# Performance work log

Measured on AMD Instinct MI355X. Metric: run time of the kernel, lower is better.

Reference implementation:

```python
import jax, jax.numpy as jnp
import numpy as np

D, N, F_IN, F_OUT = 2, 4096, 128, 128
DENSITY = 0.005  # avg degree ~20 per row in the 0/1 attention graphs
NEG_INF = -1e30


def setup_inputs() -> dict:
    key = jax.random.key(0)
    ks = jax.random.split(key, 12)
    X = jax.random.normal(ks[0], (D, N, F_IN), dtype=jnp.float32)
    # Dense Laplacian operator used in torch.sparse.mm(L[i], h_p); scaled so tanh stays non-degenerate
    L = jax.random.normal(ks[1], (D, N, N), dtype=jnp.float32) / np.float32(np.sqrt(N))
    # Upper/lower adjacency: 0/1 matrices (GATLayer extracts edges via adj == 1)
    L_u = (jax.random.uniform(ks[2], (D, N, N)) < DENSITY).astype(jnp.float32)
    L_d = (jax.random.uniform(ks[3], (D, N, N)) < DENSITY).astype(jnp.float32)
    s = np.float32(0.05)
    Wp = jax.random.normal(ks[4], (D, F_IN, F_OUT), dtype=jnp.float32) * s
    Ws = jax.random.normal(ks[5], (D, F_IN, F_OUT), dtype=jnp.float32) * s
    Wu = jax.random.normal(ks[6], (D, F_IN, F_OUT), dtype=jnp.float32) * s
    au1 = jax.random.normal(ks[7], (D, F_OUT), dtype=jnp.float32) * s
    au2 = jax.random.normal(ks[8], (D, F_OUT), dtype=jnp.float32) * s
    Wd = jax.random.normal(ks[9], (D, F_IN, F_OUT), dtype=jnp.float32) * s
    ad1 = jax.random.normal(ks[10], (D, F_OUT), dtype=jnp.float32) * s
    ad2 = jax.random.normal(ks[11], (D, F_OUT), dtype=jnp.float32) * s
    return {"X": X, "L": L, "L_u": L_u, "L_d": L_d,
            "Wp": Wp, "Ws": Ws, "Wu": Wu, "au1": au1, "au2": au2,
            "Wd": Wd, "ad1": ad1, "ad2": ad2, "dimensions": D}


def _gat(x, adj, W, a1, a2):
    # GATLayer.forward with boundary=False: linear -> edge scores -> LeakyReLU ->
    # row-wise softmax restricted to adj==1 entries -> sparse mm.
    h = x @ W                                   # [N, F_OUT]
    s1 = h @ a1                                 # [N]  (a_1 linear, bias=False)
    s2 = h @ a2                                 # [N]
    scores = jax.nn.leaky_relu(s1[:, None] + s2[None, :])  # [N, N], slope 0.01
    mask = adj == 1.0
    scores = jnp.where(mask, scores, NEG_INF)
    attn = jax.nn.softmax(scores, axis=1)
    attn = jnp.where(mask, attn, 0.0)           # zero rows with no edges (sparse softmax semantics)
    return attn @ h                             # [N, F_OUT]


def _san_dim(x, L, Lu, Ld, Wp, Ws, Wu, au1, au2, Wd, ad1, ad2):
    h_p = jnp.tanh(L @ (x @ Wp))
    h_s = jnp.tanh(x @ Ws)
    h_u = jnp.tanh(_gat(x, Lu, Wu, au1, au2))
    h_d = jnp.tanh(_gat(x, Ld, Wd, ad1, ad2))
    return h_s + h_u + h_d + h_p


def reference(X, L, L_u, L_d, Wp, Ws, Wu, au1, au2, Wd, ad1, ad2, dimensions):
    # vmap over the `dimensions` simplex levels (all per-level params stacked on axis 0)
    return jax.vmap(_san_dim)(X, L, L_u, L_d, Wp, Ws, Wu, au1, au2, Wd, ad1, ad2)
```

## Files before the change

### kernel.cpp

```cpp
#include <hip/hip_runtime.h>
#include <hip/hip_bf16.h>

#define NN 4096
#define FD 128
#define NDIM 2
#define CAP 256

typedef unsigned long long u64;

#define OFF_HMAT 0
#define OFF_SVEC 3145728
#define OFF_HP   3178496
#define OFF_H0T  7372800
#define OFF_MASK 7897088

typedef _Float16 f16x8 __attribute__((ext_vector_type(8)));
typedef float f32x4 __attribute__((ext_vector_type(4)));
typedef float f32x4v __attribute__((ext_vector_type(4)));
typedef unsigned long long u64x2 __attribute__((ext_vector_type(2)));

union P4 { _Float16 h[4]; int2 i2; };

__device__ __forceinline__ float f4get(const float4& v, int j) {
    return j == 0 ? v.x : j == 1 ? v.y : j == 2 ? v.z : v.w;
}

__global__ __launch_bounds__(256) void k_xw(
    const float* __restrict__ X, const float* __restrict__ Wp,
    const float* __restrict__ Wsm, const float* __restrict__ Wu,
    const float* __restrict__ Wd, float* __restrict__ hmat,
    _Float16* __restrict__ h0T) {
  int d = blockIdx.z, p = blockIdx.y;
  int r0 = blockIdx.x * 128;
  const float* W = (p == 0 ? Wp : p == 1 ? Wsm : p == 2 ? Wu : Wd) + (size_t)d * FD * FD;
  const float* Xd = X + ((size_t)d * NN + r0) * FD;
  __shared__ int4 As4[2048];
  __shared__ int4 Bs4[2048];
  char* As = (char*)As4; char* Bs = (char*)Bs4;
  int t = threadIdx.x;

#pragma unroll 4
  for (int u = 0; u < 16; u++) {
    int id = t + u * 256;
    int row = id >> 5, k4 = (id & 31) * 4;
    float4 v = *(const float4*)(Xd + (size_t)row * FD + k4);
    P4 pk;
    pk.h[0] = (_Float16)v.x; pk.h[1] = (_Float16)v.y;
    pk.h[2] = (_Float16)v.z; pk.h[3] = (_Float16)v.w;
    int off = (row * 256 + k4 * 2) ^ ((row & 7) << 4);
    *(int2*)(As + off) = pk.i2;
  }
#pragma unroll 4
  for (int u = 0; u < 16; u++) {
    int id = t + u * 256;
    int k = id >> 5, n4 = (id & 31) * 4;
    float4 v = *(const float4*)(W + (size_t)k * FD + n4);
#pragma unroll
    for (int j = 0; j < 4; j++) {
      int n = n4 + j;
      int off = (n * 256 + k * 2) ^ ((n & 7) << 4);
      *(_Float16*)(Bs + off) = (_Float16)f4get(v, j);
    }
  }
  __syncthreads();

  int w = t >> 6, l = t & 63;
  int lr = l & 15, lkb = (l >> 4) * 16;
  f32x4 acc[2][8] = {};
#pragma unroll
  for (int kb = 0; kb < 4; kb++) {
    f16x8 a[2], b[8];
#pragma unroll
    for (int m = 0; m < 2; m++) {
      int row = w * 32 + m * 16 + lr;
      int off = (row * 256 + kb * 64 + lkb) ^ ((row & 7) << 4);
      a[m] = *(const f16x8*)(As + off);
    }
#pragma unroll
    for (int n = 0; n < 8; n++) {
      int rn = n * 16 + lr;
      int off = (rn * 256 + kb * 64 + lkb) ^ ((rn & 7) << 4);
      b[n] = *(const f16x8*)(Bs + off);
    }
#pragma unroll
    for (int m = 0; m < 2; m++)
#pragma unroll
      for (int n = 0; n < 8; n++)
        acc[m][n] = __builtin_amdgcn_mfma_f32_16x16x32_f16(a[m], b[n], acc[m][n], 0, 0, 0);
  }

  if (p == 0) {
    _Float16* hT = h0T + (size_t)d * FD * NN;
#pragma unroll
    for (int m = 0; m < 2; m++)
#pragma unroll
      for (int n = 0; n < 8; n++) {
        int col = n * 16 + lr;
        int grow = r0 + w * 32 + m * 16 + (l >> 4) * 4;
        P4 pk;
#pragma unroll
        for (int r = 0; r < 4; r++) pk.h[r] = (_Float16)acc[m][n][r];
        *(int2*)(hT + (size_t)col * NN + grow) = pk.i2;
      }
  } else {
    float* o = hmat + ((size_t)(d * 3 + p - 1) * NN + r0) * FD;
#pragma unroll
    for (int m = 0; m < 2; m++)
#pragma unroll
      for (int n = 0; n < 8; n++)
#pragma unroll
        for (int r = 0; r < 4; r++)
          o[(size_t)(w * 32 + m * 16 + (l >> 4) * 4 + r) * FD + n * 16 + lr] = acc[m][n][r];
  }
}

__global__ __launch_bounds__(256) void k_svec(
    const float* __restrict__ hmat, const float* __restrict__ au1,
    const float* __restrict__ au2, const float* __restrict__ ad1,
    const float* __restrict__ ad2, float* __restrict__ svec) {
  int v = blockIdx.y, d = blockIdx.z;
  int w = threadIdx.x >> 6, lane = threadIdx.x & 63;
  int i = blockIdx.x * 4 + w;
  const float* a = (v == 0 ? au1 : v == 1 ? au2 : v == 2 ? ad1 : ad2) + (size_t)d * FD;
  const float* h = hmat + ((size_t)(d * 3 + 1 + (v >> 1)) * NN + i) * FD;
  float x = h[lane] * a[lane] + h[64 + lane] * a[64 + lane];
#pragma unroll
  for (int o = 1; o < 64; o <<= 1) x += __shfl_xor(x, o);
  if (lane == 0) svec[(size_t)(d * 4 + v) * NN + i] = x;
}

__global__ __launch_bounds__(256) void k_mega(
    const float* __restrict__ L, const _Float16* __restrict__ h0T,
    float* __restrict__ hp,
    const float* __restrict__ Lu, const float* __restrict__ Ldn,
    u64* __restrict__ mask) {
  __shared__ int4 sm4[1536];
  int t = threadIdx.x, w = t >> 6, lane = t & 63;

  if (blockIdx.x < 512) {
    int b = blockIdx.x;
    int r0 = (b & 63) * 64, ks = (b >> 6) & 3, d = b >> 8;
    const float* Lr = L + (size_t)d * NN * NN;
    const _Float16* hT = h0T + (size_t)d * FD * NN;
    char* As = (char*)sm4;
    char* Bs = (char*)(sm4 + 512);
    int lr = lane & 15, lkb = (lane >> 4) * 16;
    f32x4 acc[8] = {};
    int kbeg = ks * 1024;
    for (int kk = kbeg; kk < kbeg + 1024; kk += 64) {
#pragma unroll
      for (int u = 0; u < 4; u++) {
        int id = t + u * 256;
        int row = id >> 4, k4 = (id & 15) * 4;
        f32x4v v = __builtin_nontemporal_load(
            (const f32x4v*)(Lr + (size_t)(r0 + row) * NN + kk) + (k4 >> 2));
        P4 pk;
        pk.h[0] = (_Float16)v[0]; pk.h[1] = (_Float16)v[1];
        pk.h[2] = (_Float16)v[2]; pk.h[3] = (_Float16)v[3];
        int off = (row * 128 + k4 * 2) ^ ((row & 7) << 4);
        *(int2*)(As + off) = pk.i2;
      }
#pragma unroll
      for (int u = 0; u < 4; u++) {
        int id = t + u * 256;
        int n = id >> 3, k8 = (id & 7) * 8;
        int4 v = *(const int4*)(hT + (size_t)n * NN + kk + k8);
        int off = (n * 128 + k8 * 2) ^ ((n & 7) << 4);
        *(int4*)(Bs + off) = v;
      }
      __syncthreads();
#pragma unroll
      for (int kb = 0; kb < 2; kb++) {
        int row = w * 16 + lr;
        int offA = (row * 128 + kb * 64 + lkb) ^ ((row & 7) << 4);
        f16x8 a = *(const f16x8*)(As + offA);
        f16x8 bb[8];
#pragma unroll
        for (int n = 0; n < 8; n++) {
          int rn = n * 16 + lr;
          int off = (rn * 128 + kb * 64 + lkb) ^ ((rn & 7) << 4);
          bb[n] = *(const f16x8*)(Bs + off);
        }
#pragma unroll
        for (int n = 0; n < 8; n++)
          acc[n] = __builtin_amdgcn_mfma_f32_16x16x32_f16(a, bb[n], acc[n], 0, 0, 0);
      }
      __syncthreads();
    }
    float* o = hp + ((size_t)(d * 4 + ks) * NN + r0) * FD;
#pragma unroll
    for (int n = 0; n < 8; n++)
#pragma unroll
      for (int r = 0; r < 4; r++)
        o[(size_t)(w * 16 + (lane >> 4) * 4 + r) * FD + n * 16 + lr] = acc[n][r];
    return;
  }

  int hr = (blockIdx.x - 512) * 4 + w;
  int p = hr >> 13;
  int rq = hr & 8191;
  int row = rq >> 1, half = rq & 1;
  const float* src = ((p & 1) ? Ldn : Lu) +
                     ((size_t)(p >> 1) * NN + row) * (size_t)NN + half * 2048;
  f32x4v v[8];
#pragma unroll
  for (int q = 0; q < 4; q++) {
    const f32x4v* s4 = (const f32x4v*)(src + q * 512);
    v[2 * q]     = __builtin_nontemporal_load(s4 + lane);
    v[2 * q + 1] = __builtin_nontemporal_load(s4 + 64 + lane);
  }
  u64* o = mask + ((size_t)p * NN + row) * 64 + half * 32;
#pragma unroll
  for (int q = 0; q < 4; q++) {
    u64 m0 = __ballot(v[2 * q][0] == 1.0f);
    u64 m1 = __ballot(v[2 * q][1] == 1.0f);
    u64 m2 = __ballot(v[2 * q][2] == 1.0f);
    u64 m3 = __ballot(v[2 * q][3] == 1.0f);
    u64 m4 = __ballot(v[2 * q + 1][0] == 1.0f);
    u64 m5 = __ballot(v[2 * q + 1][1] == 1.0f);
    u64 m6 = __ballot(v[2 * q + 1][2] == 1.0f);
    u64 m7 = __ballot(v[2 * q + 1][3] == 1.0f);
    if (lane == 0) {
      u64x2 a0 = {m0, m1}, a1 = {m2, m3}, a2 = {m4, m5}, a3 = {m6, m7};
      __builtin_nontemporal_store(a0, (u64x2*)(o + q * 8 + 0));
      __builtin_nontemporal_store(a1, (u64x2*)(o + q * 8 + 2));
      __builtin_nontemporal_store(a2, (u64x2*)(o + q * 8 + 4));
      __builtin_nontemporal_store(a3, (u64x2*)(o + q * 8 + 6));
    }
  }
}

__global__ __launch_bounds__(256) void k_gatc(
    const u64* __restrict__ mask, const float* __restrict__ hmat,
    const float* __restrict__ svec, const float* __restrict__ hp,
    float* __restrict__ out) {
  int d = blockIdx.y;
  int w = threadIdx.x >> 6, lane = threadIdx.x & 63;
  int i = blockIdx.x * 4 + w;

  __shared__ int ej[4][2][CAP];
  __shared__ float wt[4][2][CAP];

  float ga[2][2];
#pragma unroll
  for (int a = 0; a < 2; a++) {
    const u64* mrow = mask + ((size_t)((d * 2 + a) * NN) + i) * 64;
    const float* h = hmat + (size_t)(d * 3 + 1 + a) * NN * FD;
    const float* s1 = svec + (size_t)(d * 4 + 2 * a) * NN;
    const float* s2 = svec + (size_t)(d * 4 + 2 * a + 1) * NN;

    u64 m = mrow[lane];
    int c = __popcll(m);
    int pre = c;
#pragma unroll
    for (int o = 1; o < 64; o <<= 1) {
      int tv = __shfl_up(pre, o);
      if (lane >= o) pre += tv;
    }
    int cnt = __shfl(pre, 63);
    int base = pre - c;
    int colbase = (lane >> 2) * 256 + (lane & 3);
    while (m) {
      int b = __ffsll((unsigned long long)m) - 1;
      m &= m - 1;
      if (base < CAP) ej[w][a][base] = colbase + b * 4;
      base++;
    }
    cnt = min(cnt, CAP);

    float s1i = s1[i];
    float mx = -1e30f;
    for (int e0 = 0; e0 < cnt; e0 += 64) {
      int e = e0 + lane;
      float sc = -1e30f;
      if (e < cnt) {
        int j = ej[w][a][e];
        float x = s1i + s2[j];
        sc = x > 0.0f ? x : 0.01f * x;
        wt[w][a][e] = sc;
      }
      mx = fmaxf(mx, sc);
    }
#pragma unroll
    for (int o = 1; o < 64; o <<= 1) mx = fmaxf(mx, __shfl_xor(mx, o));
    float sum = 0.0f;
    for (int e0 = 0; e0 < cnt; e0 += 64) {
      int e = e0 + lane;
      float pv = 0.0f;
      if (e < cnt) {
        pv = expf(wt[w][a][e] - mx);
        wt[w][a][e] = pv;
      }
      sum += pv;
    }
#pragma unroll
    for (int o = 1; o < 64; o <<= 1) sum += __shfl_xor(sum, o);
    float inv = (cnt > 0) ? 1.0f / sum : 0.0f;

    float acc0 = 0.0f, acc1 = 0.0f;
    int e = 0;
    for (; e + 4 <= cnt; e += 4) {
      const float* r0 = h + (size_t)ej[w][a][e + 0] * FD;
      const float* r1 = h + (size_t)ej[w][a][e + 1] * FD;
      const float* r2 = h + (size_t)ej[w][a][e + 2] * FD;
      const float* r3 = h + (size_t)ej[w][a][e + 3] * FD;
      float w0 = wt[w][a][e + 0] * inv, w1 = wt[w][a][e + 1] * inv;
      float w2 = wt[w][a][e + 2] * inv, w3 = wt[w][a][e + 3] * inv;
      float a0 = r0[lane], b0 = r0[64 + lane];
      float a1 = r1[lane], b1 = r1[64 + lane];
      float a2 = r2[lane], b2 = r2[64 + lane];
      float a3 = r3[lane], b3 = r3[64 + lane];
      acc0 += w0 * a0 + w1 * a1 + w2 * a2 + w3 * a3;
      acc1 += w0 * b0 + w1 * b1 + w2 * b2 + w3 * b3;
    }
    for (; e < cnt; e++) {
      float wg = wt[w][a][e] * inv;
      const float* hr = h + (size_t)ej[w][a][e] * FD;
      acc0 += wg * hr[lane];
      acc1 += wg * hr[64 + lane];
    }
    ga[a][0] = acc0;
    ga[a][1] = acc1;
  }

  const float* hs = hmat + ((size_t)(d * 3) * NN + i) * FD;
  const float* h0 = hp + ((size_t)(d * 4 + 0) * NN + i) * FD;
  const float* h1 = hp + ((size_t)(d * 4 + 1) * NN + i) * FD;
  const float* h2 = hp + ((size_t)(d * 4 + 2) * NN + i) * FD;
  const float* h3 = hp + ((size_t)(d * 4 + 3) * NN + i) * FD;
  float* o = out + ((size_t)d * NN + i) * FD;
#pragma unroll
  for (int hf = 0; hf < 2; hf++) {
    int col = hf * 64 + lane;
    float ps = h0[col] + h1[col] + h2[col] + h3[col];
    o[col] = tanhf(hs[col]) + tanhf(ga[0][hf]) + tanhf(ga[1][hf]) + tanhf(ps);
  }
}

extern "C" void kernel_launch(void* const* d_in, const int* in_sizes, int n_in,
                              void* d_out, int out_size, void* d_ws, size_t ws_size,
                              hipStream_t stream) {
  const float* X   = (const float*)d_in[0];
  const float* L   = (const float*)d_in[1];
  const float* Lu  = (const float*)d_in[2];
  const float* Ldn = (const float*)d_in[3];
  const float* Wp  = (const float*)d_in[4];
  const float* Wsm = (const float*)d_in[5];
  const float* Wu  = (const float*)d_in[6];
  const float* au1 = (const float*)d_in[7];
  const float* au2 = (const float*)d_in[8];
  const float* Wd  = (const float*)d_in[9];
  const float* ad1 = (const float*)d_in[10];
  const float* ad2 = (const float*)d_in[11];
  float* out = (float*)d_out;
  float* ws = (float*)d_ws;

  float* hmat = ws + OFF_HMAT;
  float* svec = ws + OFF_SVEC;
  float* hp   = ws + OFF_HP;
  _Float16* h0T = (_Float16*)(ws + OFF_H0T);
  u64* mask = (u64*)(ws + OFF_MASK);

  k_xw<<<dim3(NN / 128, 4, NDIM), 256, 0, stream>>>(X, Wp, Wsm, Wu, Wd, hmat, h0T);
  k_svec<<<dim3(NN / 4, 4, NDIM), 256, 0, stream>>>(hmat, au1, au2, ad1, ad2, svec);
  k_mega<<<dim3(512 + 8192, 1, 1), 256, 0, stream>>>(L, h0T, hp, Lu, Ldn, mask);
  k_gatc<<<dim3(NN / 4, NDIM, 1), 256, 0, stream>>>(mask, hmat, svec, hp, out);
}
```

Measured before the change: 124.5 us.

## Fuse score vectors into projection GEMM, shrink tiles, and unroll GAT gather

Computes the attention score vectors s1/s2 inside the X@W kernel epilogue with a 16-lane shuffle reduction, which removes the separate svec launch and its reread of hmat. The projection kernel now uses 64-row tiles, doubling the block count. The L@h GEMM K-step is halved to 32 to cut LDS use and raise occupancy, at the cost of twice as many barriers. The GAT aggregation hoists both mask loads and adds an 8-way unrolled gather to keep more loads in flight.

```diff
diff --git a/kernel.cpp b/kernel.cpp
--- a/kernel.cpp
+++ b/kernel.cpp
@@ -28,19 +28,21 @@
 __global__ __launch_bounds__(256) void k_xw(
     const float* __restrict__ X, const float* __restrict__ Wp,
     const float* __restrict__ Wsm, const float* __restrict__ Wu,
-    const float* __restrict__ Wd, float* __restrict__ hmat,
-    _Float16* __restrict__ h0T) {
+    const float* __restrict__ Wd, const float* __restrict__ au1,
+    const float* __restrict__ au2, const float* __restrict__ ad1,
+    const float* __restrict__ ad2, float* __restrict__ hmat,
+    _Float16* __restrict__ h0T, float* __restrict__ svec) {
   int d = blockIdx.z, p = blockIdx.y;
-  int r0 = blockIdx.x * 128;
+  int r0 = blockIdx.x * 64;
   const float* W = (p == 0 ? Wp : p == 1 ? Wsm : p == 2 ? Wu : Wd) + (size_t)d * FD * FD;
   const float* Xd = X + ((size_t)d * NN + r0) * FD;
-  __shared__ int4 As4[2048];
+  __shared__ int4 As4[1024];
   __shared__ int4 Bs4[2048];
   char* As = (char*)As4; char* Bs = (char*)Bs4;
   int t = threadIdx.x;
 
 #pragma unroll 4
-  for (int u = 0; u < 16; u++) {
+  for (int u = 0; u < 8; u++) {
     int id = t + u * 256;
     int row = id >> 5, k4 = (id & 31) * 4;
     float4 v = *(const float4*)(Xd + (size_t)row * FD + k4);
@@ -66,16 +68,13 @@
 
   int w = t >> 6, l = t & 63;
   int lr = l & 15, lkb = (l >> 4) * 16;
-  f32x4 acc[2][8] = {};
+  f32x4 acc[8] = {};
 #pragma unroll
   for (int kb = 0; kb < 4; kb++) {
-    f16x8 a[2], b[8];
-#pragma unroll
-    for (int m = 0; m < 2; m++) {
-      int row = w * 32 + m * 16 + lr;
-      int off = (row * 256 + kb * 64 + lkb) ^ ((row & 7) << 4);
-      a[m] = *(const f16x8*)(As + off);
-    }
+    int row = w * 16 + lr;
+    int offA = (row * 256 + kb * 64 + lkb) ^ ((row & 7) << 4);
+    f16x8 a = *(const f16x8*)(As + offA);
+    f16x8 b[8];
 #pragma unroll
     for (int n = 0; n < 8; n++) {
       int rn = n * 16 + lr;
@@ -83,50 +82,59 @@
       b[n] = *(const f16x8*)(Bs + off);
     }
 #pragma unroll
-    for (int m = 0; m < 2; m++)
-#pragma unroll
-      for (int n = 0; n < 8; n++)
-        acc[m][n] = __builtin_amdgcn_mfma_f32_16x16x32_f16(a[m], b[n], acc[m][n], 0, 0, 0);
+    for (int n = 0; n < 8; n++)
+      acc[n] = __builtin_amdgcn_mfma_f32_16x16x32_f16(a, b[n], acc[n], 0, 0, 0);
   }
 
   if (p == 0) {
     _Float16* hT = h0T + (size_t)d * FD * NN;
 #pragma unroll
-    for (int m = 0; m < 2; m++)
-#pragma unroll
-      for (int n = 0; n < 8; n++) {
-        int col = n * 16 + lr;
-        int grow = r0 + w * 32 + m * 16 + (l >> 4) * 4;
-        P4 pk;
-#pragma unroll
-        for (int r = 0; r < 4; r++) pk.h[r] = (_Float16)acc[m][n][r];
-        *(int2*)(hT + (size_t)col * NN + grow) = pk.i2;
-      }
+    for (int n = 0; n < 8; n++) {
+      int col = n * 16 + lr;
+      int grow = r0 + w * 16 + (l >> 4) * 4;
+      P4 pk;
+#pragma unroll
+      for (int r = 0; r < 4; r++) pk.h[r] = (_Float16)acc[n][r];
+      *(int2*)(hT + (size_t)col * NN + grow) = pk.i2;
+    }
   } else {
     float* o = hmat + ((size_t)(d * 3 + p - 1) * NN + r0) * FD;
 #pragma unroll
-    for (int m = 0; m < 2; m++)
-#pragma unroll
-      for (int n = 0; n < 8; n++)
-#pragma unroll
-        for (int r = 0; r < 4; r++)
-          o[(size_t)(w * 32 + m * 16 + (l >> 4) * 4 + r) * FD + n * 16 + lr] = acc[m][n][r];
-  }
-}
-
-__global__ __launch_bounds__(256) void k_svec(
-    const float* __restrict__ hmat, const float* __restrict__ au1,
-    const float* __restrict__ au2, const float* __restrict__ ad1,
-    const float* __restrict__ ad2, float* __restrict__ svec) {
-  int v = blockIdx.y, d = blockIdx.z;
-  int w = threadIdx.x >> 6, lane = threadIdx.x & 63;
-  int i = blockIdx.x * 4 + w;
-  const float* a = (v == 0 ? au1 : v == 1 ? au2 : v == 2 ? ad1 : ad2) + (size_t)d * FD;
-  const float* h = hmat + ((size_t)(d * 3 + 1 + (v >> 1)) * NN + i) * FD;
-  float x = h[lane] * a[lane] + h[64 + lane] * a[64 + lane];
-#pragma unroll
-  for (int o = 1; o < 64; o <<= 1) x += __shfl_xor(x, o);
-  if (lane == 0) svec[(size_t)(d * 4 + v) * NN + i] = x;
+    for (int n = 0; n < 8; n++)
+#pragma unroll
+      for (int r = 0; r < 4; r++)
+        o[(size_t)(w * 16 + (l >> 4) * 4 + r) * FD + n * 16 + lr] = acc[n][r];
+    if (p >= 2) {
+      const float* a1 = (p == 2 ? au1 : ad1) + (size_t)d * FD;
+      const float* a2 = (p == 2 ? au2 : ad2) + (size_t)d * FD;
+      float av1[8], av2[8];
+#pragma unroll
+      for (int n = 0; n < 8; n++) {
+        av1[n] = a1[n * 16 + lr];
+        av2[n] = a2[n * 16 + lr];
+      }
+      int vb = (d * 4 + (p - 2) * 2);
+#pragma unroll
+      for (int r = 0; r < 4; r++) {
+        float p1 = 0.0f, p2 = 0.0f;
+#pragma unroll
+        for (int n = 0; n < 8; n++) {
+          p1 += acc[n][r] * av1[n];
+          p2 += acc[n][r] * av2[n];
+        }
+#pragma unroll
+        for (int o2 = 1; o2 < 16; o2 <<= 1) {
+          p1 += __shfl_xor(p1, o2);
+          p2 += __shfl_xor(p2, o2);
+        }
+        if (lr == 0) {
+          int row = r0 + w * 16 + (l >> 4) * 4 + r;
+          svec[(size_t)vb * NN + row] = p1;
+          svec[(size_t)(vb + 1) * NN + row] = p2;
+        }
+      }
+    }
+  }
 }
 
 __global__ __launch_bounds__(256) void k_mega(
@@ -134,7 +142,7 @@
     float* __restrict__ hp,
     const float* __restrict__ Lu, const float* __restrict__ Ldn,
     u64* __restrict__ mask) {
-  __shared__ int4 sm4[1536];
+  __shared__ int4 sm4[768];
   int t = threadIdx.x, w = t >> 6, lane = t & 63;
 
   if (blockIdx.x < 512) {
@@ -143,42 +151,41 @@
     const float* Lr = L + (size_t)d * NN * NN;
     const _Float16* hT = h0T + (size_t)d * FD * NN;
     char* As = (char*)sm4;
-    char* Bs = (char*)(sm4 + 512);
+    char* Bs = (char*)(sm4 + 256);
     int lr = lane & 15, lkb = (lane >> 4) * 16;
     f32x4 acc[8] = {};
     int kbeg = ks * 1024;
-    for (int kk = kbeg; kk < kbeg + 1024; kk += 64) {
-#pragma unroll
-      for (int u = 0; u < 4; u++) {
+    for (int kk = kbeg; kk < kbeg + 1024; kk += 32) {
+#pragma unroll
+      for (int u = 0; u < 2; u++) {
         int id = t + u * 256;
-        int row = id >> 4, k4 = (id & 15) * 4;
+        int row = id >> 3, k4 = (id & 7) * 4;
         f32x4v v = __builtin_nontemporal_load(
             (const f32x4v*)(Lr + (size_t)(r0 + row) * NN + kk) + (k4 >> 2));
         P4 pk;
         pk.h[0] = (_Float16)v[0]; pk.h[1] = (_Float16)v[1];
         pk.h[2] = (_Float16)v[2]; pk.h[3] = (_Float16)v[3];
-        int off = (row * 128 + k4 * 2) ^ ((row & 7) << 4);
+        int off = (row * 64 + k4 * 2) ^ ((row & 3) << 4);
         *(int2*)(As + off) = pk.i2;
       }
 #pragma unroll
-      for (int u = 0; u < 4; u++) {
+      for (int u = 0; u < 2; u++) {
         int id = t + u * 256;
-        int n = id >> 3, k8 = (id & 7) * 8;
+        int n = id >> 2, k8 = (id & 3) * 8;
         int4 v = *(const int4*)(hT + (size_t)n * NN + kk + k8);
-        int off = (n * 128 + k8 * 2) ^ ((n & 7) << 4);
+        int off = (n * 64 + k8 * 2) ^ ((n & 3) << 4);
         *(int4*)(Bs + off) = v;
       }
       __syncthreads();
-#pragma unroll
-      for (int kb = 0; kb < 2; kb++) {
+      {
         int row = w * 16 + lr;
-        int offA = (row * 128 + kb * 64 + lkb) ^ ((row & 7) << 4);
+        int offA = (row * 64 + lkb) ^ ((row & 3) << 4);
         f16x8 a = *(const f16x8*)(As + offA);
         f16x8 bb[8];
 #pragma unroll
         for (int n = 0; n < 8; n++) {
           int rn = n * 16 + lr;
-          int off = (rn * 128 + kb * 64 + lkb) ^ ((rn & 7) << 4);
+          int off = (rn * 64 + lkb) ^ ((rn & 3) << 4);
           bb[n] = *(const f16x8*)(Bs + off);
         }
 #pragma unroll
@@ -241,15 +248,17 @@
   __shared__ int ej[4][2][CAP];
   __shared__ float wt[4][2][CAP];
 
+  u64 mm0 = mask[((size_t)((d * 2 + 0) * NN) + i) * 64 + lane];
+  u64 mm1 = mask[((size_t)((d * 2 + 1) * NN) + i) * 64 + lane];
+
   float ga[2][2];
 #pragma unroll
   for (int a = 0; a < 2; a++) {
-    const u64* mrow = mask + ((size_t)((d * 2 + a) * NN) + i) * 64;
     const float* h = hmat + (size_t)(d * 3 + 1 + a) * NN * FD;
     const float* s1 = svec + (size_t)(d * 4 + 2 * a) * NN;
     const float* s2 = svec + (size_t)(d * 4 + 2 * a + 1) * NN;
 
-    u64 m = mrow[lane];
+    u64 m = a == 0 ? mm0 : mm1;
     int c = __popcll(m);
     int pre = c;
 #pragma unroll
@@ -299,6 +308,26 @@
 
     float acc0 = 0.0f, acc1 = 0.0f;
     int e = 0;
+    for (; e + 8 <= cnt; e += 8) {
+      const float* rp[8];
+      float wg[8];
+#pragma unroll
+      for (int q = 0; q < 8; q++) {
+        rp[q] = h + (size_t)ej[w][a][e + q] * FD;
+        wg[q] = wt[w][a][e + q] * inv;
+      }
+      float va[8], vb[8];
+#pragma unroll
+      for (int q = 0; q < 8; q++) {
+        va[q] = rp[q][lane];
+        vb[q] = rp[q][64 + lane];
+      }
+#pragma unroll
+      for (int q = 0; q < 8; q++) {
+        acc0 += wg[q] * va[q];
+        acc1 += wg[q] * vb[q];
+      }
+    }
     for (; e + 4 <= cnt; e += 4) {
       const float* r0 = h + (size_t)ej[w][a][e + 0] * FD;
       const float* r1 = h + (size_t)ej[w][a][e + 1] * FD;
@@ -306,12 +335,8 @@
       const float* r3 = h + (size_t)ej[w][a][e + 3] * FD;
       float w0 = wt[w][a][e + 0] * inv, w1 = wt[w][a][e + 1] * inv;
       float w2 = wt[w][a][e + 2] * inv, w3 = wt[w][a][e + 3] * inv;
-      float a0 = r0[lane], b0 = r0[64 + lane];
-      float a1 = r1[lane], b1 = r1[64 + lane];
-      float a2 = r2[lane], b2 = r2[64 + lane];
-      float a3 = r3[lane], b3 = r3[64 + lane];
-      acc0 += w0 * a0 + w1 * a1 + w2 * a2 + w3 * a3;
-      acc1 += w0 * b0 + w1 * b1 + w2 * b2 + w3 * b3;
+      acc0 += w0 * r0[lane] + w1 * r1[lane] + w2 * r2[lane] + w3 * r3[lane];
+      acc1 += w0 * r0[64 + lane] + w1 * r1[64 + lane] + w2 * r2[64 + lane] + w3 * r3[64 + lane];
     }
     for (; e < cnt; e++) {
       float wg = wt[w][a][e] * inv;
@@ -361,8 +386,8 @@
   _Float16* h0T = (_Float16*)(ws + OFF_H0T);
   u64* mask = (u64*)(ws + OFF_MASK);
 
-  k_xw<<<dim3(NN / 128, 4, NDIM), 256, 0, stream>>>(X, Wp, Wsm, Wu, Wd, hmat, h0T);
-  k_svec<<<dim3(NN / 4, 4, NDIM), 256, 0, stream>>>(hmat, au1, au2, ad1, ad2, svec);
+  k_xw<<<dim3(NN / 64, 4, NDIM), 256, 0, stream>>>(
+      X, Wp, Wsm, Wu, Wd, au1, au2, ad1, ad2, hmat, h0T, svec);
   k_mega<<<dim3(512 + 8192, 1, 1), 256, 0, stream>>>(L, h0T, hp, Lu, Ldn, mask);
   k_gatc<<<dim3(NN / 4, NDIM, 1), 256, 0, stream>>>(mask, hmat, svec, hp, out);
 }
```

Result: slower. 130.2 us (+4.6%).
